# Kernel optimization log

Hardware: AMD Instinct MI355X
Metric: run time of the kernel (lower is better)

## Reference

```python
import jax, jax.numpy as jnp
import numpy as np

B, C, N, O, K = 4, 64, 8192, 128, 20


def setup_inputs() -> dict:
    key = jax.random.key(0)
    k1, k2, k3 = jax.random.split(key, 3)
    x = jax.random.normal(k1, (B, C, N), dtype=jnp.float32)
    # Conv2d(2C, 2C, 1, bias=False) weight squeezed to [2C, 2C]
    W1 = jax.random.normal(k2, (2 * C, 2 * C), dtype=jnp.float32) * (1.0 / np.sqrt(2 * C))
    # Conv2d(2C, O, 1, bias=False) weight squeezed to [O, 2C]
    W2 = jax.random.normal(k3, (O, 2 * C), dtype=jnp.float32) * (1.0 / np.sqrt(2 * C))
    return {"x": x, "W1": W1, "W2": W2, "spiral_size": K}


def _knn_idx(x, k):
    # x: [B, C, N]; negative squared pairwise distance, top-k = k nearest (incl. self)
    inner = -2.0 * jnp.einsum('bcn,bcm->bnm', x, x)          # [B, N, N]
    xx = jnp.sum(x * x, axis=1)                               # [B, N]
    pd = -xx[:, :, None] - inner - xx[:, None, :]             # [B, N, N]
    return jax.lax.top_k(pd, k)[1]                            # [B, N, k] int32


def reference(x, W1, W2, spiral_size):
    b, c, n = x.shape
    idx = _knn_idx(x, spiral_size)                            # [B, N, K]
    xt = jnp.transpose(x, (0, 2, 1))                          # [B, N, C]
    spirals = xt[jnp.arange(b)[:, None, None], idx]           # [B, N, K, C] neighbor gather
    center = jnp.broadcast_to(xt[:, :, None, :], spirals.shape)
    feats = jnp.concatenate([spirals - center, center], axis=-1)  # [B, N, K, 2C]
    h = jnp.einsum('bnkc,dc->bnkd', feats, W1)                # 1x1 conv1
    gate = jax.nn.softmax(h, axis=2)                          # softmax over neighbor dim K
    gated = feats * gate                                      # [B, N, K, 2C]
    out = jnp.einsum('bnkc,oc->bon', gated, W2)               # conv2 + sum over K -> [B, O, N]
    return out
```

## Files before the change

### kernel.cpp

```cpp
#include <hip/hip_runtime.h>
#include <math.h>

#define BB 4
#define CC 64
#define NN 8192
#define OO 128
#define KK 20
#define DD 128
#define NCH 2
#define CH (NN / NCH)
#define TC 32
#define NT (CH / TC)
#define BUFSZ 8

typedef short bf16x8 __attribute__((ext_vector_type(8)));
typedef float f32x4 __attribute__((ext_vector_type(4)));
typedef unsigned short u16x8 __attribute__((ext_vector_type(8)));
typedef unsigned long long u64;

typedef __attribute__((address_space(1))) const void gvoid;
typedef __attribute__((address_space(3))) void lvoid;

__device__ __forceinline__ u64 packkey(float v, int idx) {
  unsigned u = __float_as_uint(v);
  unsigned o = ((int)u < 0) ? ~u : (u | 0x80000000u);
  return (((u64)o) << 32) | (unsigned)(~idx);
}
__device__ __forceinline__ float keyval(u64 k) {
  unsigned o = (unsigned)(k >> 32);
  unsigned u = (o & 0x80000000u) ? (o ^ 0x80000000u) : ~o;
  return __uint_as_float(u);
}
#define INITKEY (((u64)0x007FFFFFu) << 32)

__device__ __forceinline__ unsigned short bf_rne(float f) {
  unsigned u = __float_as_uint(f);
  u += 0x7FFFu + ((u >> 16) & 1u);
  return (unsigned short)(u >> 16);
}
__device__ __forceinline__ float bf_f(unsigned short h) {
  return __uint_as_float(((unsigned)h) << 16);
}

__global__ __launch_bounds__(128) void prep_kernel(const float* __restrict__ x,
                                                   float* __restrict__ xx,
                                                   unsigned short* __restrict__ xs) {
  const int tid = threadIdx.x;
  const int b = blockIdx.y;
  const int n0 = blockIdx.x * 128;
  const float* xb = x + (size_t)b * CC * NN;
  float xv[CC];
  float acc = 0.0f;
  #pragma unroll
  for (int c = 0; c < CC; ++c) {
    float v = xb[(size_t)c * NN + n0 + tid];
    acc += v * v;
    xv[c] = v;
  }
  xx[b * NN + n0 + tid] = acc;

  const int n = n0 + tid;
  char* xsrow = ((char*)xs) + ((size_t)b * NN + n) * 384;
  const int swn = (n & 7) << 4;
  #pragma unroll
  for (int gr = 0; gr < 8; ++gr) {
    u16x8 h8, m8, l8;
    #pragma unroll
    for (int e = 0; e < 8; ++e) {
      float v = xv[gr * 8 + e];
      unsigned short h = bf_rne(v);
      float r = v - bf_f(h);
      unsigned short m = bf_rne(r);
      r -= bf_f(m);
      unsigned short l = bf_rne(r);
      h8[e] = (unsigned short)h; m8[e] = m; l8[e] = l;
    }
    *(u16x8*)(xsrow + (((gr * 16) + 0) ^ swn)) = h8;
    *(u16x8*)(xsrow + (((gr * 16) + 128) ^ swn)) = m8;
    *(u16x8*)(xsrow + (((gr * 16) + 256) ^ swn)) = l8;
  }
}

__global__ __launch_bounds__(256, 4) void knn_kernel(
    const unsigned short* __restrict__ xs, const float* __restrict__ xx,
    u64* __restrict__ pkeys) {
  __shared__ __attribute__((aligned(16))) unsigned short atile[TC * 192];
  __shared__ __attribute__((aligned(16))) char bufmem[4 * 64 * BUFSZ * 6];
  __shared__ float cxx[TC];
  float* pdb = (float*)bufmem;
  unsigned short* idb = (unsigned short*)(bufmem + 4 * 64 * BUFSZ * 4);

  const int tid = threadIdx.x;
  const int w = tid >> 6;
  const int lane = tid & 63;
  const int r = lane & 15;
  const int g = lane >> 4;
  const int lin = blockIdx.x;
  const int xcd = lin & 7;
  const int b = xcd >> 1;
  const int ch = xcd & 1;
  const int qg = lin >> 3;
  const int qbase = qg * 64 + w * 16;
  const int q = qbase + r;
  const int cbase = ch * CH;
  const char* xsb = ((const char*)xs) + (size_t)b * NN * 384;

  bf16x8 bq[3][2];
  {
    const char* qrow = xsb + (size_t)q * 384;
    const int sw = (q & 7) << 4;
    #pragma unroll
    for (int s = 0; s < 3; ++s)
      #pragma unroll
      for (int c = 0; c < 2; ++c)
        bq[s][c] = *(const bf16x8*)(qrow + ((s * 128 + c * 64 + g * 16) ^ sw));
  }
  const float xxq = xx[b * NN + q];

  u64 tk[KK];
  #pragma unroll
  for (int j = 0; j < KK; ++j) tk[j] = INITKEY;
  float minv = -INFINITY;
  int cnt = 0;
  float* pdl = pdb + (w * 64 + lane) * BUFSZ;
  unsigned short* idl = idb + (w * 64 + lane) * BUFSZ;

  auto stage = [&](int t) {
    const char* src = xsb + (size_t)(cbase + t * TC) * 384;
    char* dst = (char*)atile;
    #pragma unroll
    for (int it = 0; it < 3; ++it) {
      __builtin_amdgcn_global_load_lds(
          (gvoid*)(src + it * 4096 + tid * 16),
          (lvoid*)(dst + it * 4096 + tid * 16), 16, 0, 0);
    }
    if (tid < 8)
      __builtin_amdgcn_global_load_lds(
          (gvoid*)(xx + b * NN + cbase + t * TC + tid * 4),
          (lvoid*)(cxx + tid * 4), 16, 0, 0);
  };

  auto rebuild = [&]() {
    int mxc = cnt;
    #pragma unroll
    for (int o = 32; o > 0; o >>= 1) {
      int v = __shfl_xor(mxc, o);
      mxc = mxc > v ? mxc : v;
    }
    for (int i = 0; i < mxc; ++i) {
      u64 k = (i < cnt) ? packkey(pdl[i], (int)idl[i]) : 0ULL;
      if (k > tk[KK - 1]) {
        #pragma unroll
        for (int jj = KK - 1; jj >= 1; --jj)
          tk[jj] = (k > tk[jj - 1]) ? tk[jj - 1] : ((k > tk[jj]) ? k : tk[jj]);
        tk[0] = (k > tk[0]) ? k : tk[0];
      }
    }
    cnt = 0;
    minv = keyval(tk[KK - 1]);
  };

  for (int t = 0; t < NT; ++t) {
    stage(t);
    __syncthreads();

    #pragma unroll
    for (int ct = 0; ct < 2; ++ct) {
      const char* arow = ((const char*)atile) + (ct * 16 + r) * 384;
      const int sw = (r & 7) << 4;
      bf16x8 a6[6];
      #pragma unroll
      for (int c6 = 0; c6 < 6; ++c6)
        a6[c6] = *(const bf16x8*)(arow + ((c6 * 64 + g * 16) ^ sw));
      f32x4 acc = {0.f, 0.f, 0.f, 0.f};
      __builtin_amdgcn_s_setprio(1);
      #pragma unroll
      for (int s = 2; s >= 0; --s)
        #pragma unroll
        for (int c6 = 0; c6 < 6; ++c6)
          acc = __builtin_amdgcn_mfma_f32_16x16x32_bf16(a6[c6], bq[s][c6 & 1],
                                                        acc, 0, 0, 0);
      __builtin_amdgcn_s_setprio(0);

      float pd0 = (-xxq - (-2.0f * acc[0])) - cxx[ct * 16 + g * 4 + 0];
      float pd1 = (-xxq - (-2.0f * acc[1])) - cxx[ct * 16 + g * 4 + 1];
      float pd2 = (-xxq - (-2.0f * acc[2])) - cxx[ct * 16 + g * 4 + 2];
      float pd3 = (-xxq - (-2.0f * acc[3])) - cxx[ct * 16 + g * 4 + 3];
      const float maxpd = fmaxf(fmaxf(pd0, pd1), fmaxf(pd2, pd3));
      if (__any(maxpd > minv)) {
        const int i0 = cbase + t * TC + ct * 16 + g * 4;
        if (pd0 > minv) { pdl[cnt] = pd0; idl[cnt] = (unsigned short)(i0 + 0); ++cnt; }
        if (pd1 > minv) { pdl[cnt] = pd1; idl[cnt] = (unsigned short)(i0 + 1); ++cnt; }
        if (pd2 > minv) { pdl[cnt] = pd2; idl[cnt] = (unsigned short)(i0 + 2); ++cnt; }
        if (pd3 > minv) { pdl[cnt] = pd3; idl[cnt] = (unsigned short)(i0 + 3); ++cnt; }
        if (__any(cnt > BUFSZ - 4)) rebuild();
      }
    }
    __syncthreads();
  }

  rebuild();

  for (int pass = 0; pass < 2; ++pass) {
    __syncthreads();
    if ((w >> 1) == pass) {
      u64* ml = (w & 1) ? (u64*)bufmem : (u64*)atile;
      #pragma unroll
      for (int j = 0; j < KK; ++j) ml[lane * KK + j] = tk[j];
      if (lane < 16) {
        u64* po = pkeys + (((size_t)b * NN + qbase + lane) * NCH + ch) * KK;
        const u64* L0 = ml + (lane + 0) * KK;
        const u64* L1 = ml + (lane + 16) * KK;
        const u64* L2 = ml + (lane + 32) * KK;
        const u64* L3 = ml + (lane + 48) * KK;
        int p0 = 0, p1 = 0, p2 = 0, p3 = 0;
        u64 h0 = L0[0], h1 = L1[0], h2 = L2[0], h3 = L3[0];
        #pragma unroll
        for (int k = 0; k < KK; ++k) {
          u64 bv = h0; int bc = 0;
          if (h1 > bv) { bv = h1; bc = 1; }
          if (h2 > bv) { bv = h2; bc = 2; }
          if (h3 > bv) { bv = h3; bc = 3; }
          po[k] = bv;
          if (bc == 0)      { ++p0; h0 = (p0 < KK) ? L0[p0] : 0ULL; }
          else if (bc == 1) { ++p1; h1 = (p1 < KK) ? L1[p1] : 0ULL; }
          else if (bc == 2) { ++p2; h2 = (p2 < KK) ? L2[p2] : 0ULL; }
          else              { ++p3; h3 = (p3 < KK) ? L3[p3] : 0ULL; }
        }
      }
    }
  }
}

__global__ __launch_bounds__(256) void merge_kernel(const u64* __restrict__ pkeys,
                                                    int* __restrict__ fidx) {
  const int q = blockIdx.x * 256 + threadIdx.x;
  const u64* pk = pkeys + (size_t)q * NCH * KK;
  int* fo = fidx + (size_t)q * KK;
  int p0 = 0, p1 = 0;
  u64 h0 = pk[0], h1 = pk[KK];
  #pragma unroll
  for (int k = 0; k < KK; ++k) {
    const bool t1 = h1 > h0;
    const u64 bv = t1 ? h1 : h0;
    fo[k] = (int)(~(unsigned)bv);
    if (t1) { ++p1; h1 = (p1 < KK) ? pk[KK + p1] : 0ULL; }
    else    { ++p0; h0 = (p0 < KK) ? pk[p0] : 0ULL; }
  }
}

__global__ __launch_bounds__(256) void w1prep_kernel(const float* __restrict__ W1,
                                                     unsigned short* __restrict__ w1p) {
  for (int e = threadIdx.x; e < 12288; e += 256) {
    const int f = e >> 9;
    const int rr = e & 511;
    const int l = rr >> 3;
    const int j = rr & 7;
    const int pair = f / 3, s = f % 3;
    const int dt = pair >> 1, kc = pair & 1;
    const int d = dt * 16 + (l & 15);
    const int c = kc * 32 + (l >> 4) * 8 + j;
    const float v = W1[d * DD + c];
    const unsigned short h = bf_rne(v);
    float r = v - bf_f(h);
    const unsigned short m = bf_rne(r);
    r -= bf_f(m);
    const unsigned short lo = bf_rne(r);
    w1p[(size_t)f * 512 + l * 8 + j] = (s == 0) ? h : ((s == 1) ? m : lo);
  }
}

#define MFMA16(A, B, C) __builtin_amdgcn_mfma_f32_16x16x32_bf16((A), (B), (C), 0, 0, 0)

template <int SA, int SB>
__device__ __forceinline__ void h_term(const bf16x8 (&a)[3][2][2],
                                       const bf16x8 (&w1f)[24],
                                       f32x4 (&acc)[4][2]) {
  #pragma unroll
  for (int dt = 0; dt < 4; ++dt)
    #pragma unroll
    for (int kc = 0; kc < 2; ++kc) {
      const bf16x8 bf = w1f[(dt * 2 + kc) * 3 + SB];
      acc[dt][0] = MFMA16(a[SA][kc][0], bf, acc[dt][0]);
      acc[dt][1] = MFMA16(a[SA][kc][1], bf, acc[dt][1]);
    }
}

template <int DT>
__device__ __forceinline__ float d1_epi(const bf16x8 (&a)[3][2][2],
                                        bf16x8 id0, bf16x8 id1,
                                        const f32x4 (&acc)[4][2], int g) {
  constexpr int KC = DT >> 1;
  const bf16x8 idp = (DT & 1) ? id1 : id0;
  f32x4 yf0 = {0.f, 0.f, 0.f, 0.f}, yf1 = {0.f, 0.f, 0.f, 0.f};
  yf0 = MFMA16(a[1][KC][0], idp, yf0);
  yf0 = MFMA16(a[0][KC][0], idp, yf0);
  yf1 = MFMA16(a[1][KC][1], idp, yf1);
  yf1 = MFMA16(a[0][KC][1], idp, yf1);
  const f32x4 h0 = acc[DT][0], h1 = acc[DT][1];
  float mx = fmaxf(fmaxf(h0[0], h0[1]), fmaxf(h0[2], h0[3]));
  mx = fmaxf(mx, fmaxf(fmaxf(h1[0], h1[1]), fmaxf(h1[2], h1[3])));
  mx = fmaxf(mx, __shfl_xor(mx, 16));
  mx = fmaxf(mx, __shfl_xor(mx, 32));
  float sl = 0.f, tl = 0.f;
  #pragma unroll
  for (int j = 0; j < 4; ++j) {
    const float e = __expf(h0[j] - mx);
    sl += e; tl += yf0[j] * e;
  }
  if (g == 0) {
    #pragma unroll
    for (int j = 0; j < 4; ++j) {
      const float e = __expf(h1[j] - mx);
      sl += e; tl += yf1[j] * e;
    }
  }
  sl += __shfl_xor(sl, 16); sl += __shfl_xor(sl, 32);
  tl += __shfl_xor(tl, 16); tl += __shfl_xor(tl, 32);
  return tl / sl;
}

__global__ __launch_bounds__(256, 2) void d1_kernel(
    const unsigned short* __restrict__ xs, const int* __restrict__ fidx,
    const unsigned short* __restrict__ w1p, float* __restrict__ gbuf) {
  const int tid = threadIdx.x;
  const int w = tid >> 6;
  const int lane = tid & 63;
  const int r = lane & 15;
  const int g = lane >> 4;
  const int b = blockIdx.y;
  const char* xsb = ((const char*)xs) + (size_t)b * NN * 384;

  bf16x8 w1f[24];
  #pragma unroll
  for (int f = 0; f < 24; ++f)
    w1f[f] = *(const bf16x8*)(((const char*)w1p) + f * 1024 + lane * 16);

  bf16x8 id0, id1;
  #pragma unroll
  for (int j = 0; j < 8; ++j) {
    id0[j] = (g == (r >> 3) && j == (r & 7)) ? (short)0x3F80 : (short)0;
    id1[j] = (g == 2 + (r >> 3) && j == (r & 7)) ? (short)0x3F80 : (short)0;
  }

  for (int i = 0; i < 4; ++i) {
    const int n = blockIdx.x * 16 + w * 4 + i;
    const size_t ng = (size_t)b * NN + n;
    const int* kp = fidx + ng * KK;
    const int row0 = kp[r];
    const int row1 = kp[16 + (r & 3)];
    const char* rp0 = xsb + (size_t)row0 * 384;
    const char* rp1 = xsb + (size_t)row1 * 384;
    const int sw0 = (row0 & 7) << 4, sw1 = (row1 & 7) << 4;

    bf16x8 a[3][2][2];
    #pragma unroll
    for (int s = 0; s < 3; ++s)
      #pragma unroll
      for (int kc = 0; kc < 2; ++kc) {
        const int off = s * 128 + kc * 64 + g * 16;
        a[s][kc][0] = *(const bf16x8*)(rp0 + (off ^ sw0));
        a[s][kc][1] = *(const bf16x8*)(rp1 + (off ^ sw1));
      }

    const char* zrow = xsb + (size_t)n * 384;
    const int swn = (n & 7) << 4;
    float zl;
    {
      const unsigned short zh = *(const unsigned short*)(zrow + ((2 * lane) ^ swn));
      const unsigned short zm = *(const unsigned short*)(zrow + ((128 + 2 * lane) ^ swn));
      const unsigned short zo = *(const unsigned short*)(zrow + ((256 + 2 * lane) ^ swn));
      zl = bf_f(zh) + bf_f(zm) + bf_f(zo);
    }

    f32x4 acc[4][2];
    #pragma unroll
    for (int dt = 0; dt < 4; ++dt) {
      acc[dt][0] = (f32x4){0.f, 0.f, 0.f, 0.f};
      acc[dt][1] = (f32x4){0.f, 0.f, 0.f, 0.f};
    }
    h_term<2, 0>(a, w1f, acc);
    h_term<0, 2>(a, w1f, acc);
    h_term<1, 1>(a, w1f, acc);
    h_term<1, 0>(a, w1f, acc);
    h_term<0, 1>(a, w1f, acc);
    h_term<0, 0>(a, w1f, acc);

    const float t0 = d1_epi<0>(a, id0, id1, acc, g);
    const float t1 = d1_epi<1>(a, id0, id1, acc, g);
    const float t2 = d1_epi<2>(a, id0, id1, acc, g);
    const float t3 = d1_epi<3>(a, id0, id1, acc, g);

    float* go = gbuf + ng * DD;
    go[64 + lane] = zl;
    const float z0 = __shfl(zl, r);
    const float z1 = __shfl(zl, 16 + r);
    const float z2 = __shfl(zl, 32 + r);
    const float z3 = __shfl(zl, 48 + r);
    if (lane < 16) {
      go[r]      = t0 - z0;
      go[16 + r] = t1 - z1;
      go[32 + r] = t2 - z2;
      go[48 + r] = t3 - z3;
    }
  }
}

__global__ __launch_bounds__(256) void d2_kernel(const float* __restrict__ gbuf,
                                                 const float* __restrict__ W2,
                                                 float* __restrict__ out) {
  __shared__ float4 w2s[OO * 32];
  const int tid = threadIdx.x;
  const int b = blockIdx.y;
  const int n0 = blockIdx.x * 32;
  const float4* w2v = (const float4*)W2;
  for (int t = tid; t < OO * 32; t += 256) {
    int o = t >> 5, c4 = t & 31;
    w2s[o * 32 + (c4 ^ (o & 7))] = w2v[t];
  }
  __syncthreads();
  const int og = tid & 7;
  const int ni = tid >> 3;
  const int n = n0 + ni;
  const float4* gp = (const float4*)(gbuf + ((size_t)b * NN + n) * DD);
  float acc[16];
  #pragma unroll
  for (int j = 0; j < 16; ++j) acc[j] = 0.0f;
  for (int c4 = 0; c4 < 32; ++c4) {
    float4 g4 = gp[c4];
    #pragma unroll
    for (int j = 0; j < 16; ++j) {
      const int o = j * 8 + og;
      float4 w4 = w2s[o * 32 + (c4 ^ og)];
      acc[j] += g4.x * w4.x + g4.y * w4.y + g4.z * w4.z + g4.w * w4.w;
    }
  }
  float* outb = out + (size_t)b * OO * NN;
  #pragma unroll
  for (int j = 0; j < 16; ++j) {
    outb[(size_t)(j * 8 + og) * NN + n] = acc[j];
  }
}

extern "C" void kernel_launch(void* const* d_in, const int* in_sizes, int n_in,
                              void* d_out, int out_size, void* d_ws, size_t ws_size,
                              hipStream_t stream) {
  const float* x  = (const float*)d_in[0];
  const float* W1 = (const float*)d_in[1];
  const float* W2 = (const float*)d_in[2];
  float* out = (float*)d_out;
  char* ws = (char*)d_ws;
  unsigned short* xs = (unsigned short*)(ws);
  float* xx = (float*)(ws + 12582912);
  unsigned short* w1p = (unsigned short*)(ws + 12582912);
  int* fidx = (int*)(ws + 12713984);
  u64* pkeys = (u64*)(ws + 15335424);
  float* gbuf = (float*)(ws + 15335424);

  prep_kernel<<<dim3(NN / 128, BB), 128, 0, stream>>>(x, xx, xs);
  knn_kernel<<<dim3(1024), 256, 0, stream>>>(xs, xx, pkeys);
  merge_kernel<<<dim3(BB * NN / 256), 256, 0, stream>>>(pkeys, fidx);
  w1prep_kernel<<<dim3(1), 256, 0, stream>>>(W1, w1p);
  d1_kernel<<<dim3(NN / 16, BB), 256, 0, stream>>>(xs, fidx, w1p, gbuf);
  d2_kernel<<<dim3(NN / 32, BB), 256, 0, stream>>>(gbuf, W2, out);
}
```

Baseline: 790.1 us.

## Double kNN candidate tile and transpose per-lane LDS buffers to avoid bank conflicts

```diff
diff --git a/kernel.cpp b/kernel.cpp
--- a/kernel.cpp
+++ b/kernel.cpp
@@ -9,7 +9,7 @@
 #define DD 128
 #define NCH 2
 #define CH (NN / NCH)
-#define TC 32
+#define TC 64
 #define NT (CH / TC)
 #define BUFSZ 8
 
@@ -20,6 +20,8 @@
 
 typedef __attribute__((address_space(1))) const void gvoid;
 typedef __attribute__((address_space(3))) void lvoid;
+
+#define MFMA16(A, B, C) __builtin_amdgcn_mfma_f32_16x16x32_bf16((A), (B), (C), 0, 0, 0)
 
 __device__ __forceinline__ u64 packkey(float v, int idx) {
   unsigned u = __float_as_uint(v);
@@ -85,10 +87,10 @@
     const unsigned short* __restrict__ xs, const float* __restrict__ xx,
     u64* __restrict__ pkeys) {
   __shared__ __attribute__((aligned(16))) unsigned short atile[TC * 192];
-  __shared__ __attribute__((aligned(16))) char bufmem[4 * 64 * BUFSZ * 6];
+  __shared__ __attribute__((aligned(16))) char bufmem[12288];
   __shared__ float cxx[TC];
   float* pdb = (float*)bufmem;
-  unsigned short* idb = (unsigned short*)(bufmem + 4 * 64 * BUFSZ * 4);
+  unsigned short* idb = (unsigned short*)(bufmem + 8192);
 
   const int tid = threadIdx.x;
   const int w = tid >> 6;
@@ -117,24 +119,34 @@
   }
   const float xxq = xx[b * NN + q];
 
+  int aoff[4][6];
+  {
+    const int sw = (r & 7) << 4;
+    #pragma unroll
+    for (int ct = 0; ct < 4; ++ct)
+      #pragma unroll
+      for (int c6 = 0; c6 < 6; ++c6)
+        aoff[ct][c6] = (ct * 16 + r) * 384 + ((c6 * 64 + g * 16) ^ sw);
+  }
+
   u64 tk[KK];
   #pragma unroll
   for (int j = 0; j < KK; ++j) tk[j] = INITKEY;
   float minv = -INFINITY;
   int cnt = 0;
-  float* pdl = pdb + (w * 64 + lane) * BUFSZ;
-  unsigned short* idl = idb + (w * 64 + lane) * BUFSZ;
+  float* pdl = pdb + w * (BUFSZ * 64) + lane;
+  unsigned short* idl = idb + w * (BUFSZ * 64) + lane;
 
   auto stage = [&](int t) {
     const char* src = xsb + (size_t)(cbase + t * TC) * 384;
     char* dst = (char*)atile;
     #pragma unroll
-    for (int it = 0; it < 3; ++it) {
+    for (int it = 0; it < 6; ++it) {
       __builtin_amdgcn_global_load_lds(
           (gvoid*)(src + it * 4096 + tid * 16),
           (lvoid*)(dst + it * 4096 + tid * 16), 16, 0, 0);
     }
-    if (tid < 8)
+    if (tid < 16)
       __builtin_amdgcn_global_load_lds(
           (gvoid*)(xx + b * NN + cbase + t * TC + tid * 4),
           (lvoid*)(cxx + tid * 4), 16, 0, 0);
@@ -148,7 +160,7 @@
       mxc = mxc > v ? mxc : v;
     }
     for (int i = 0; i < mxc; ++i) {
-      u64 k = (i < cnt) ? packkey(pdl[i], (int)idl[i]) : 0ULL;
+      u64 k = (i < cnt) ? packkey(pdl[i * 64], (int)idl[i * 64]) : 0ULL;
       if (k > tk[KK - 1]) {
         #pragma unroll
         for (int jj = KK - 1; jj >= 1; --jj)
@@ -165,21 +177,18 @@
     __syncthreads();
 
     #pragma unroll
-    for (int ct = 0; ct < 2; ++ct) {
-      const char* arow = ((const char*)atile) + (ct * 16 + r) * 384;
-      const int sw = (r & 7) << 4;
+    for (int ct = 0; ct < 4; ++ct) {
       bf16x8 a6[6];
       #pragma unroll
       for (int c6 = 0; c6 < 6; ++c6)
-        a6[c6] = *(const bf16x8*)(arow + ((c6 * 64 + g * 16) ^ sw));
+        a6[c6] = *(const bf16x8*)(((const char*)atile) + aoff[ct][c6]);
       f32x4 acc = {0.f, 0.f, 0.f, 0.f};
       __builtin_amdgcn_s_setprio(1);
       #pragma unroll
       for (int s = 2; s >= 0; --s)
         #pragma unroll
         for (int c6 = 0; c6 < 6; ++c6)
-          acc = __builtin_amdgcn_mfma_f32_16x16x32_bf16(a6[c6], bq[s][c6 & 1],
-                                                        acc, 0, 0, 0);
+          acc = MFMA16(a6[c6], bq[s][c6 & 1], acc);
       __builtin_amdgcn_s_setprio(0);
 
       float pd0 = (-xxq - (-2.0f * acc[0])) - cxx[ct * 16 + g * 4 + 0];
@@ -189,10 +198,10 @@
       const float maxpd = fmaxf(fmaxf(pd0, pd1), fmaxf(pd2, pd3));
       if (__any(maxpd > minv)) {
         const int i0 = cbase + t * TC + ct * 16 + g * 4;
-        if (pd0 > minv) { pdl[cnt] = pd0; idl[cnt] = (unsigned short)(i0 + 0); ++cnt; }
-        if (pd1 > minv) { pdl[cnt] = pd1; idl[cnt] = (unsigned short)(i0 + 1); ++cnt; }
-        if (pd2 > minv) { pdl[cnt] = pd2; idl[cnt] = (unsigned short)(i0 + 2); ++cnt; }
-        if (pd3 > minv) { pdl[cnt] = pd3; idl[cnt] = (unsigned short)(i0 + 3); ++cnt; }
+        if (pd0 > minv) { pdl[cnt * 64] = pd0; idl[cnt * 64] = (unsigned short)(i0 + 0); ++cnt; }
+        if (pd1 > minv) { pdl[cnt * 64] = pd1; idl[cnt * 64] = (unsigned short)(i0 + 1); ++cnt; }
+        if (pd2 > minv) { pdl[cnt * 64] = pd2; idl[cnt * 64] = (unsigned short)(i0 + 2); ++cnt; }
+        if (pd3 > minv) { pdl[cnt * 64] = pd3; idl[cnt * 64] = (unsigned short)(i0 + 3); ++cnt; }
         if (__any(cnt > BUFSZ - 4)) rebuild();
       }
     }
@@ -270,8 +279,6 @@
   }
 }
 
-#define MFMA16(A, B, C) __builtin_amdgcn_mfma_f32_16x16x32_bf16((A), (B), (C), 0, 0, 0)
-
 template <int SA, int SB>
 __device__ __forceinline__ void h_term(const bf16x8 (&a)[3][2][2],
                                        const bf16x8 (&w1f)[24],
```

Measured after the change: 706.2 us, median of 2. -10.6%, faster.
